# Optimization experiments

Hardware: AMD Instinct MI355X
Metric: run time of the kernel (lower is better)

## Reference

```python
import jax, jax.numpy as jnp
import numpy as np

T = 4096
C = 2048
N_FEAT = 2048
NEG = -1e30  # finite stand-in for -inf so fully-masked (padding) rows stay NaN-free


def setup_inputs() -> dict:
    key = jax.random.key(0)
    kx, kw, kb = jax.random.split(key, 3)
    x = jax.random.normal(kx, (T, C), dtype=jnp.float32)
    # Dense(features=3*n_feat): kernel (C, 3*n_feat), bias (3*n_feat,)
    W = jax.random.normal(kw, (C, 3 * N_FEAT), dtype=jnp.float32) * (1.0 / np.sqrt(C))
    b = jax.random.normal(kb, (3 * N_FEAT,), dtype=jnp.float32) * 0.01
    n_padd = 128
    return {"x": x, "W": W, "b": b, "n_padd": n_padd}


def reference(x, W, b, n_padd):
    T_, _ = x.shape
    qkv = x @ W + b                      # (T, 3*n_feat)
    q, k, v = jnp.split(qkv, 3, axis=1)  # each (T, n_feat)
    scale = 1.0 / jnp.sqrt(jnp.float32(q.shape[1]))
    att = (q @ k.T) * scale              # (T, T)
    rows = jnp.arange(T_)[:, None]
    cols = jnp.arange(T_)[None, :]
    # causal AND both row/col past the left padding
    mask = (cols <= rows) & (cols >= n_padd) & (rows >= n_padd)
    att = jnp.where(mask, att, NEG)
    p = jax.nn.softmax(att, axis=1)      # stable row softmax
    # kernel only stores rows >= n_padd; padding rows are zero
    p = jnp.where(rows >= n_padd, p, 0.0)
    y = p @ v                            # (T, n_feat)
    return y
```

## Files before the change

kernel.cpp:

```cpp
#include <hip/hip_runtime.h>
#include <cstdint>


#define T_DIM 4096
#define C_DIM 2048
#define NF    2048
#define N3    6144
#define NEGV  (-1e30f)

typedef __bf16 bf16x8 __attribute__((ext_vector_type(8)));
typedef __bf16 bf16x4 __attribute__((ext_vector_type(4)));
typedef float  f32x4  __attribute__((ext_vector_type(4)));

__device__ __forceinline__ void async_cp16(const void* g, void* l) {
    __builtin_amdgcn_global_load_lds(
        reinterpret_cast<const __attribute__((address_space(1))) unsigned int*>(
            reinterpret_cast<uintptr_t>(g)),
        reinterpret_cast<__attribute__((address_space(3))) unsigned int*>(
            reinterpret_cast<uintptr_t>(l)),
        16, 0, 0);
}

__device__ __forceinline__ void gemm_loop(const __bf16* A, const __bf16* B,
                                          int lda, int ldb, int m0, int n0,
                                          int kiters, __bf16* As, __bf16* Bs,
                                          f32x4 (&acc)[4][4]) {
    const int t    = threadIdx.x;
    const int wv   = t >> 6;
    const int lane = t & 63;
    const int srow = t >> 3;
    const int scol = (((t & 7) ^ (srow & 7)) << 3);
    const int wm   = (wv >> 1) << 6;
    const int wn   = (wv & 1) << 6;
    const int lrow = lane & 15;
    const int kq   = lane >> 4;
    const int swz  = lrow & 7;
    const int rc0  = ((kq ^ swz) << 3);
    const int rc1  = (((kq | 4) ^ swz) << 3);

    const __bf16* ga = A + (size_t)(m0 + srow) * lda + scol;
    const __bf16* gb = B + (size_t)(n0 + srow) * ldb + scol;

    for (int kk = 0; kk < kiters; ++kk) {
#pragma unroll
        for (int i = 0; i < 4; ++i) {
            async_cp16(ga + (size_t)(32 * i) * lda, &As[i * 2048 + wv * 512]);
            async_cp16(gb + (size_t)(32 * i) * ldb, &Bs[i * 2048 + wv * 512]);
        }
        ga += 64; gb += 64;
        __syncthreads();

#pragma unroll
        for (int kb = 0; kb < 2; ++kb) {
            const int rc = kb ? rc1 : rc0;
            bf16x8 af[4], bfr[4];
#pragma unroll
            for (int mi = 0; mi < 4; ++mi)
                af[mi] = *(const bf16x8*)&As[(wm + mi * 16 + lrow) * 64 + rc];
#pragma unroll
            for (int ni = 0; ni < 4; ++ni)
                bfr[ni] = *(const bf16x8*)&Bs[(wn + ni * 16 + lrow) * 64 + rc];
#pragma unroll
            for (int mi = 0; mi < 4; ++mi)
#pragma unroll
                for (int ni = 0; ni < 4; ++ni)
                    acc[mi][ni] = __builtin_amdgcn_mfma_f32_16x16x32_bf16(
                        af[mi], bfr[ni], acc[mi][ni], 0, 0, 0);
        }
        __syncthreads();
    }
}

__global__ void cast_x_kernel(const float* __restrict__ x,
                              __bf16* __restrict__ xb, int n4) {
    int stride = gridDim.x * blockDim.x;
    for (int i = blockIdx.x * blockDim.x + threadIdx.x; i < n4; i += stride) {
        float4 v = ((const float4*)x)[i];
        bf16x4 o;
        o[0] = (__bf16)v.x; o[1] = (__bf16)v.y;
        o[2] = (__bf16)v.z; o[3] = (__bf16)v.w;
        ((bf16x4*)xb)[i] = o;
    }
}

__global__ void transpose_w_kernel(const float* __restrict__ W,
                                   __bf16* __restrict__ Wt) {
    __shared__ float tile[32][33];
    int bx = blockIdx.x * 32;
    int by = blockIdx.y * 32;
    int tx = threadIdx.x, ty = threadIdx.y;
#pragma unroll
    for (int i = 0; i < 32; i += 8)
        tile[ty + i][tx] = W[(size_t)(by + ty + i) * N3 + bx + tx];
    __syncthreads();
#pragma unroll
    for (int i = 0; i < 32; i += 8)
        Wt[(size_t)(bx + ty + i) * C_DIM + by + tx] = (__bf16)tile[tx][ty + i];
}

#define EPILOG_SETUP()                                     \
    const int t = threadIdx.x, wv = t >> 6, lane = t & 63; \
    const int wm = (wv >> 1) << 6, wn = (wv & 1) << 6;     \
    const int rq = (lane >> 4) << 2, cn = lane & 15

__global__ void __launch_bounds__(256)
qkv_gemm_kernel(const __bf16* __restrict__ xb, const __bf16* __restrict__ Wt,
                const float* __restrict__ bias, __bf16* __restrict__ qb,
                __bf16* __restrict__ kb, __bf16* __restrict__ vT) {
    __shared__ __bf16 As[128 * 64];
    __shared__ __bf16 Bs[128 * 64];
    f32x4 acc[4][4] = {};
    const int m0 = blockIdx.x * 128, n0 = blockIdx.y * 128;
    gemm_loop(xb, Wt, C_DIM, C_DIM, m0, n0, C_DIM / 64, As, Bs, acc);

    EPILOG_SETUP();
#pragma unroll
    for (int mi = 0; mi < 4; ++mi)
#pragma unroll
        for (int ni = 0; ni < 4; ++ni) {
            int col = n0 + wn + ni * 16 + cn;
            float bv = bias[col];
#pragma unroll
            for (int r = 0; r < 4; ++r) {
                int row = m0 + wm + mi * 16 + rq + r;
                float val = acc[mi][ni][r] + bv;
                if (col < NF)
                    qb[(size_t)row * NF + col] = (__bf16)val;
                else if (col < 2 * NF)
                    kb[(size_t)row * NF + (col - NF)] = (__bf16)val;
                else
                    vT[(size_t)(col - 2 * NF) * T_DIM + row] = (__bf16)val;
            }
        }
}

__global__ void __launch_bounds__(256)
sc_gemm_kernel(const __bf16* __restrict__ qb, const __bf16* __restrict__ kb,
               __bf16* __restrict__ S, const int* __restrict__ npadd_p) {
    int i = blockIdx.x;
    int mt = (int)((sqrtf(8.0f * (float)i + 1.0f) - 1.0f) * 0.5f);
    while ((mt + 1) * (mt + 2) / 2 <= i) ++mt;
    while (mt * (mt + 1) / 2 > i) --mt;
    int nt = i - mt * (mt + 1) / 2;
    const int m0 = mt * 128, n0 = nt * 128;
    const int npadd = *npadd_p;
    if (m0 + 128 <= npadd || n0 + 128 <= npadd) return;

    __shared__ __bf16 As[128 * 64];
    __shared__ __bf16 Bs[128 * 64];
    f32x4 acc[4][4] = {};
    gemm_loop(qb, kb, NF, NF, m0, n0, NF / 64, As, Bs, acc);

    const float scale = 0.022097086912079608f;
    EPILOG_SETUP();
#pragma unroll
    for (int mi = 0; mi < 4; ++mi)
#pragma unroll
        for (int ni = 0; ni < 4; ++ni) {
            int j = n0 + wn + ni * 16 + cn;
#pragma unroll
            for (int r = 0; r < 4; ++r) {
                int row = m0 + wm + mi * 16 + rq + r;
                S[(size_t)row * T_DIM + j] = (__bf16)(acc[mi][ni][r] * scale);
            }
        }
}

__global__ void __launch_bounds__(256)
softmax_kernel(const __bf16* __restrict__ S, __bf16* __restrict__ P,
               const int* __restrict__ npadd_p) {
    const int wv = threadIdx.x >> 6, lane = threadIdx.x & 63;
    const int row = blockIdx.x * 4 + wv;
    const int npadd = *npadd_p;
    __bf16* prow = P + (size_t)row * T_DIM;

    if (row < npadd) {
        bf16x8 z = {};
#pragma unroll
        for (int c = 0; c < 8; ++c) ((bf16x8*)prow)[c * 64 + lane] = z;
        return;
    }

    const __bf16* srow = S + (size_t)row * T_DIM;
    float vals[64];
    float mx = NEGV;
#pragma unroll
    for (int c = 0; c < 8; ++c) {
        if (c * 512 > row) {
#pragma unroll
            for (int e = 0; e < 8; ++e) vals[c * 8 + e] = NEGV;
            continue;
        }
        int j0 = c * 512 + lane * 8;
        bf16x8 v = ((const bf16x8*)srow)[c * 64 + lane];
#pragma unroll
        for (int e = 0; e < 8; ++e) {
            float f = (j0 + e >= npadd && j0 + e <= row) ? (float)v[e] : NEGV;
            vals[c * 8 + e] = f;
            mx = fmaxf(mx, f);
        }
    }
#pragma unroll
    for (int o = 32; o > 0; o >>= 1) mx = fmaxf(mx, __shfl_xor(mx, o));

    float sm = 0.f;
#pragma unroll
    for (int k = 0; k < 64; ++k) {
        vals[k] = exp2f((vals[k] - mx) * 1.4426950408889634f);
        sm += vals[k];
    }
#pragma unroll
    for (int o = 32; o > 0; o >>= 1) sm += __shfl_xor(sm, o);
    float inv = 1.0f / sm;

#pragma unroll
    for (int c = 0; c < 8; ++c) {
        bf16x8 o;
#pragma unroll
        for (int e = 0; e < 8; ++e) o[e] = (__bf16)(vals[c * 8 + e] * inv);
        ((bf16x8*)prow)[c * 64 + lane] = o;
    }
}

__global__ void __launch_bounds__(256)
pv_gemm_kernel(const __bf16* __restrict__ P, const __bf16* __restrict__ vT,
               float* __restrict__ out, const int* __restrict__ npadd_p) {
    const int idx = blockIdx.x;
    const int j = idx & 255, h = idx >> 8;
    int mt = j >> 3; if (h) mt = 31 - mt;
    const int nt = (j & 7) + (h << 3);
    const int m0 = mt * 128, n0 = nt * 128;
    const int kskip = *npadd_p >> 6;
    const int kiters = (mt + 1) * 2 - kskip;

    __shared__ __bf16 As[128 * 64];
    __shared__ __bf16 Bs[128 * 64];
    f32x4 acc[4][4] = {};
    gemm_loop(P + (size_t)kskip * 64, vT + (size_t)kskip * 64,
              T_DIM, T_DIM, m0, n0, kiters, As, Bs, acc);

    EPILOG_SETUP();
#pragma unroll
    for (int mi = 0; mi < 4; ++mi)
#pragma unroll
        for (int ni = 0; ni < 4; ++ni) {
            int col = n0 + wn + ni * 16 + cn;
#pragma unroll
            for (int r = 0; r < 4; ++r) {
                int row = m0 + wm + mi * 16 + rq + r;
                out[(size_t)row * NF + col] = acc[mi][ni][r];
            }
        }
}

extern "C" void kernel_launch(void* const* d_in, const int* in_sizes, int n_in,
                              void* d_out, int out_size, void* d_ws,
                              size_t ws_size, hipStream_t stream) {
    const float* x = (const float*)d_in[0];
    const float* W = (const float*)d_in[1];
    const float* b = (const float*)d_in[2];
    const int* npadd = (const int*)d_in[3];
    float* out = (float*)d_out;

    char* ws = (char*)d_ws;
    __bf16* xb = (__bf16*)(ws);
    __bf16* Wt = (__bf16*)(ws + (16ull << 20));
    __bf16* qb = (__bf16*)(ws + (40ull << 20));
    __bf16* kb = (__bf16*)(ws + (56ull << 20));
    __bf16* vT = (__bf16*)(ws + (72ull << 20));
    __bf16* S  = (__bf16*)(ws + (88ull << 20));
    __bf16* P  = (__bf16*)(ws + (40ull << 20));

    cast_x_kernel<<<2048, 256, 0, stream>>>(x, xb, (T_DIM * C_DIM) / 4);
    transpose_w_kernel<<<dim3(N3 / 32, C_DIM / 32), dim3(32, 8), 0, stream>>>(W, Wt);
    qkv_gemm_kernel<<<dim3(T_DIM / 128, N3 / 128), 256, 0, stream>>>(xb, Wt, b,
                                                                     qb, kb, vT);
    sc_gemm_kernel<<<528, 256, 0, stream>>>(qb, kb, S, npadd);
    softmax_kernel<<<T_DIM / 4, 256, 0, stream>>>(S, P, npadd);
    pv_gemm_kernel<<<512, 256, 0, stream>>>(P, vT, out, npadd);
}
```

Baseline: 376.8 us.

## Split-K the long PV rows with atomics, fuse prep kernels, vectorize vT stores

The lower half of the PV GEMM rows, which have the longest causal K range, is split into two K halves that accumulate into a zeroed output with atomic adds. This evens out per-block work and raises the block count from 512 to 768. The x cast and W transpose are merged into one launch, and the transposed V epilogue writes four contiguous bf16 values at once instead of scalars. The costs are an extra memset, atomic traffic on half of the output, and summation order that is no longer deterministic.

```diff
diff --git a/kernel.cpp b/kernel.cpp
--- a/kernel.cpp
+++ b/kernel.cpp
@@ -71,24 +71,27 @@
     }
 }
 
-__global__ void cast_x_kernel(const float* __restrict__ x,
-                              __bf16* __restrict__ xb, int n4) {
-    int stride = gridDim.x * blockDim.x;
-    for (int i = blockIdx.x * blockDim.x + threadIdx.x; i < n4; i += stride) {
-        float4 v = ((const float4*)x)[i];
-        bf16x4 o;
-        o[0] = (__bf16)v.x; o[1] = (__bf16)v.y;
-        o[2] = (__bf16)v.z; o[3] = (__bf16)v.w;
-        ((bf16x4*)xb)[i] = o;
-    }
-}
-
-__global__ void transpose_w_kernel(const float* __restrict__ W,
-                                   __bf16* __restrict__ Wt) {
+__global__ void prep_kernel(const float* __restrict__ x,
+                            __bf16* __restrict__ xb,
+                            const float* __restrict__ W,
+                            __bf16* __restrict__ Wt) {
+    if (blockIdx.x < 2048) {
+        const int n4 = (T_DIM * C_DIM) / 4;
+        const int stride = 2048 * 256;
+        for (int i = blockIdx.x * 256 + threadIdx.x; i < n4; i += stride) {
+            float4 v = ((const float4*)x)[i];
+            bf16x4 o;
+            o[0] = (__bf16)v.x; o[1] = (__bf16)v.y;
+            o[2] = (__bf16)v.z; o[3] = (__bf16)v.w;
+            ((bf16x4*)xb)[i] = o;
+        }
+        return;
+    }
     __shared__ float tile[32][33];
-    int bx = blockIdx.x * 32;
-    int by = blockIdx.y * 32;
-    int tx = threadIdx.x, ty = threadIdx.y;
+    const int tb = blockIdx.x - 2048;
+    const int bx = (tb % (N3 / 32)) * 32;
+    const int by = (tb / (N3 / 32)) * 32;
+    const int tx = threadIdx.x & 31, ty = threadIdx.x >> 5;
 #pragma unroll
     for (int i = 0; i < 32; i += 8)
         tile[ty + i][tx] = W[(size_t)(by + ty + i) * N3 + bx + tx];
@@ -120,16 +123,22 @@
         for (int ni = 0; ni < 4; ++ni) {
             int col = n0 + wn + ni * 16 + cn;
             float bv = bias[col];
-#pragma unroll
-            for (int r = 0; r < 4; ++r) {
-                int row = m0 + wm + mi * 16 + rq + r;
-                float val = acc[mi][ni][r] + bv;
-                if (col < NF)
-                    qb[(size_t)row * NF + col] = (__bf16)val;
-                else if (col < 2 * NF)
-                    kb[(size_t)row * NF + (col - NF)] = (__bf16)val;
-                else
-                    vT[(size_t)(col - 2 * NF) * T_DIM + row] = (__bf16)val;
+            if (col >= 2 * NF) {
+                bf16x4 o;
+#pragma unroll
+                for (int r = 0; r < 4; ++r) o[r] = (__bf16)(acc[mi][ni][r] + bv);
+                int row = m0 + wm + mi * 16 + rq;
+                *(bf16x4*)&vT[(size_t)(col - 2 * NF) * T_DIM + row] = o;
+            } else {
+#pragma unroll
+                for (int r = 0; r < 4; ++r) {
+                    int row = m0 + wm + mi * 16 + rq + r;
+                    float val = acc[mi][ni][r] + bv;
+                    if (col < NF)
+                        qb[(size_t)row * NF + col] = (__bf16)val;
+                    else
+                        kb[(size_t)row * NF + (col - NF)] = (__bf16)val;
+                }
             }
         }
 }
@@ -226,18 +235,30 @@
 pv_gemm_kernel(const __bf16* __restrict__ P, const __bf16* __restrict__ vT,
                float* __restrict__ out, const int* __restrict__ npadd_p) {
     const int idx = blockIdx.x;
-    const int j = idx & 255, h = idx >> 8;
-    int mt = j >> 3; if (h) mt = 31 - mt;
-    const int nt = (j & 7) + (h << 3);
+    const int kskip = *npadd_p >> 6;
+    int mt, nt, start, iters;
+    bool atomic_out;
+    if (idx < 256) {
+        mt = idx & 15; nt = idx >> 4;
+        int kt = (mt + 1) * 2 - kskip; if (kt < 0) kt = 0;
+        start = kskip; iters = kt; atomic_out = false;
+    } else {
+        int j = idx - 256;
+        mt = 16 + (j & 15); nt = (j >> 4) & 15;
+        int half = j >> 8;
+        int kt = (mt + 1) * 2 - kskip; if (kt < 0) kt = 0;
+        int h0 = (kt + 1) >> 1;
+        start = kskip + (half ? h0 : 0);
+        iters = half ? kt - h0 : h0;
+        atomic_out = true;
+    }
     const int m0 = mt * 128, n0 = nt * 128;
-    const int kskip = *npadd_p >> 6;
-    const int kiters = (mt + 1) * 2 - kskip;
 
     __shared__ __bf16 As[128 * 64];
     __shared__ __bf16 Bs[128 * 64];
     f32x4 acc[4][4] = {};
-    gemm_loop(P + (size_t)kskip * 64, vT + (size_t)kskip * 64,
-              T_DIM, T_DIM, m0, n0, kiters, As, Bs, acc);
+    gemm_loop(P + (size_t)start * 64, vT + (size_t)start * 64,
+              T_DIM, T_DIM, m0, n0, iters, As, Bs, acc);
 
     EPILOG_SETUP();
 #pragma unroll
@@ -248,7 +269,9 @@
 #pragma unroll
             for (int r = 0; r < 4; ++r) {
                 int row = m0 + wm + mi * 16 + rq + r;
-                out[(size_t)row * NF + col] = acc[mi][ni][r];
+                float* p = &out[(size_t)row * NF + col];
+                if (atomic_out) unsafeAtomicAdd(p, acc[mi][ni][r]);
+                else            *p = acc[mi][ni][r];
             }
         }
 }
@@ -271,11 +294,12 @@
     __bf16* S  = (__bf16*)(ws + (88ull << 20));
     __bf16* P  = (__bf16*)(ws + (40ull << 20));
 
-    cast_x_kernel<<<2048, 256, 0, stream>>>(x, xb, (T_DIM * C_DIM) / 4);
-    transpose_w_kernel<<<dim3(N3 / 32, C_DIM / 32), dim3(32, 8), 0, stream>>>(W, Wt);
+    hipMemsetAsync(out + (size_t)2048 * NF, 0, (size_t)2048 * NF * 4, stream);
+
+    prep_kernel<<<2048 + (N3 / 32) * (C_DIM / 32), 256, 0, stream>>>(x, xb, W, Wt);
     qkv_gemm_kernel<<<dim3(T_DIM / 128, N3 / 128), 256, 0, stream>>>(xb, Wt, b,
                                                                      qb, kb, vT);
     sc_gemm_kernel<<<528, 256, 0, stream>>>(qb, kb, S, npadd);
     softmax_kernel<<<T_DIM / 4, 256, 0, stream>>>(S, P, npadd);
-    pv_gemm_kernel<<<512, 256, 0, stream>>>(P, vT, out, npadd);
-}
+    pv_gemm_kernel<<<768, 256, 0, stream>>>(P, vT, out, npadd);
+}
```

Result: faster. 354.1 us (-6.0%).
